# Kernel tuning notes

Hardware: AMD Instinct MI355X
Metric: run time of the kernel (lower is better)

Reference implementation:

```python
import jax, jax.numpy as jnp
import numpy as np

N_DIM = 128
M_SEQ = 2048
BATCH = 256


def setup_inputs() -> dict:
    key = jax.random.key(0)
    k1, k2, k3 = jax.random.split(key, 3)
    scale = 1.0 / np.sqrt(N_DIM)
    return {
        "x": jax.random.normal(k1, (BATCH, N_DIM, M_SEQ), dtype=jnp.float32),
        "W": jax.random.normal(k2, (N_DIM, 3 * N_DIM), dtype=jnp.float32) * scale,
        "U": jax.random.normal(k3, (N_DIM, 3 * N_DIM), dtype=jnp.float32) * scale,
        "b": jnp.zeros((3 * N_DIM,), dtype=jnp.float32),
    }


def reference(x, W, U, b):
    # x: [B, D, T] -> scan over T with a GRU cell, output [B, D, T]
    B, D, T = x.shape
    xs = jnp.transpose(x, (2, 0, 1))  # [T, B, D]

    def cell(h, xt):
        gx = xt @ W + b              # [B, 3D]
        gh = h @ U                   # [B, 3D]
        xz, xr, xn = jnp.split(gx, 3, axis=-1)
        hz, hr, hn = jnp.split(gh, 3, axis=-1)
        z = jax.nn.sigmoid(xz + hz)  # update gate
        r = jax.nn.sigmoid(xr + hr)  # reset gate
        n = jnp.tanh(xn + r * hn)    # candidate
        h_new = z * h + (1.0 - z) * n
        return h_new, h_new

    h0 = jnp.zeros((B, D), dtype=x.dtype)
    _, ys = jax.lax.scan(cell, h0, xs)   # ys: [T, B, D]
    return jnp.transpose(ys, (1, 2, 0))  # [B, D, T]
```

## Files before the change

kernel.cpp:

```cpp
#include <hip/hip_runtime.h>

typedef float f32x4 __attribute__((ext_vector_type(4)));
typedef short bf16x8 __attribute__((ext_vector_type(8)));

#define TT    2048
#define DDIM  128
#define G3    384
#define NBBLK 16
#define GXROW 6144
#define GX_BYTES ((size_t)NBBLK * TT * GXROW * 2)

#define SCL_ZR (-1.4426950408889634f)
#define SCL_N  (-2.8853900817779268f)

__device__ __forceinline__ unsigned f2bf_u(float f) {
    unsigned u = __float_as_uint(f);
    return (u + 0x7FFFu + ((u >> 16) & 1u)) >> 16;
}
__device__ __forceinline__ float bf_lo(unsigned u) { return __uint_as_float(u << 16); }
__device__ __forceinline__ float bf_hi(unsigned u) { return __uint_as_float(u & 0xffff0000u); }
__device__ __forceinline__ float rcp_(float x) { return __builtin_amdgcn_rcpf(x); }
__device__ __forceinline__ float exp2_(float x) {
    float d;
    asm("v_exp_f32 %0, %1" : "=v"(d) : "v"(x));
    return d;
}
__device__ __forceinline__ float sigm_(float v) { return rcp_(1.0f + exp2_(-1.4426950408889634f * v)); }
__device__ __forceinline__ float tanhf_(float v) { return 2.0f * rcp_(1.0f + exp2_(-2.8853900817779268f * v)) - 1.0f; }
__device__ __forceinline__ unsigned cvt_pk_bf16(float lo, float hi) {
    unsigned d;
    asm("v_cvt_pk_bf16_f32 %0, %1, %2" : "=v"(d) : "v"(lo), "v"(hi));
    return d;
}

__global__ __launch_bounds__(256) void gx_gemm(
    const float* __restrict__ x, const float* __restrict__ W,
    const float* __restrict__ bias, unsigned short* __restrict__ gx)
{
    const int bblk  = blockIdx.x;
    const int ttile = blockIdx.y;
    const int tid = threadIdx.x;
    const int w  = tid >> 6;
    const int l  = tid & 63;
    const int lc = l & 15;
    const int lk = l >> 4;

    __shared__ unsigned short xs[16 * 16 * DDIM];

    const int tiles[6] = {2*w, 2*w+1, 2*w+8, 2*w+9, 2*w+16, 2*w+17};

    bf16x8 wfrag[6][4];
    f32x4  binit[6];
    #pragma unroll
    for (int i6 = 0; i6 < 6; ++i6) {
        const float scl = (i6 >= 4) ? SCL_N : SCL_ZR;
        #pragma unroll
        for (int i = 0; i < 4; ++i)
            binit[i6][i] = bias[tiles[i6] * 16 + lk * 4 + i] * scl;
        #pragma unroll
        for (int kt = 0; kt < 4; ++kt) {
            bf16x8 f;
            #pragma unroll
            for (int jj = 0; jj < 8; ++jj) {
                const int k = kt * 32 + lk * 8 + jj;
                f[jj] = (short)f2bf_u(W[k * G3 + tiles[i6] * 16 + lc] * scl);
            }
            wfrag[i6][kt] = f;
        }
    }

    int inoff[4];
    #pragma unroll
    for (int kt = 0; kt < 4; ++kt)
        inoff[kt] = (lc * 256 + kt * 64 + lk * 16) ^ ((lc & 7) << 4);

    const float* xb = x + (size_t)bblk * 16 * DDIM * TT;
    const int t0blk = ttile * 128;
    const int tq = tid & 3;
    const int pbase = tid >> 2;

    for (int chunk = 0; chunk < 8; ++chunk) {
        __syncthreads();
        const int t0 = t0blk + chunk * 16 + tq * 4;
        #pragma unroll 4
        for (int pp = 0; pp < 32; ++pp) {
            const int p = pbase + pp * 64;
            const int r = p >> 7, d = p & 127;
            f32x4 v = *(const f32x4*)(xb + (size_t)p * TT + t0);
            char* bp = (char*)xs + (tq * 4) * 4096 + (((r * 128 + d) * 2) ^ ((r & 7) << 4));
            const unsigned pkA = cvt_pk_bf16(v[0], v[1]);
            const unsigned pkB = cvt_pk_bf16(v[2], v[3]);
            *(unsigned short*)(bp)         = (unsigned short)pkA;
            *(unsigned short*)(bp + 4096)  = (unsigned short)(pkA >> 16);
            *(unsigned short*)(bp + 8192)  = (unsigned short)pkB;
            *(unsigned short*)(bp + 12288) = (unsigned short)(pkB >> 16);
        }
        __syncthreads();

        for (int t = 0; t < 16; ++t) {
            bf16x8 a[4];
            #pragma unroll
            for (int kt = 0; kt < 4; ++kt)
                a[kt] = *(const bf16x8*)((const char*)xs + t * 4096 + inoff[kt]);

            const int tglob = t0blk + chunk * 16 + t;
            #pragma unroll
            for (int i6 = 0; i6 < 6; ++i6) {
                f32x4 acc = binit[i6];
                #pragma unroll
                for (int kt = 0; kt < 4; ++kt)
                    acc = __builtin_amdgcn_mfma_f32_16x16x32_bf16(wfrag[i6][kt], a[kt], acc, 0, 0, 0);
                unsigned p0 = cvt_pk_bf16(acc[0], acc[1]);
                unsigned p1 = cvt_pk_bf16(acc[2], acc[3]);
                const size_t off = (size_t)(bblk * TT + tglob) * GXROW
                                   + (size_t)(((tiles[i6] * 4 + lk) * 16 + lc) * 4);
                *(uint2*)(gx + off) = make_uint2(p0, p1);
            }
        }
    }
}

__global__ __launch_bounds__(512, 2) void gru_rec(
    const unsigned short* __restrict__ gx, const float* __restrict__ U,
    float* __restrict__ out)
{
    const int bblk = blockIdx.x;
    const int tid  = threadIdx.x;
    const int w  = tid >> 6;
    const int l  = tid & 63;
    const int lc = l & 15, lk = l >> 4;

    bf16x8 uz[4], ur[4], un[4];
    #pragma unroll
    for (int kt = 0; kt < 4; ++kt) {
        bf16x8 fz, fr, fn;
        #pragma unroll
        for (int jj = 0; jj < 8; ++jj) {
            const int k = kt * 32 + lk * 8 + jj;
            fz[jj] = (short)f2bf_u(U[k * G3 + (w * 16 + lc)] * SCL_ZR);
            fr[jj] = (short)f2bf_u(U[k * G3 + 128 + (w * 16 + lc)] * SCL_ZR);
            fn[jj] = (short)f2bf_u(U[k * G3 + 256 + (w * 16 + lc)] * SCL_N);
        }
        uz[kt] = fz; ur[kt] = fr; un[kt] = fn;
    }

    __shared__ unsigned short hsA[2 * 2048];
    __shared__ float hlds[16 * 16 * 128];
    #pragma unroll
    for (int i = tid; i < 4096; i += 512) hsA[i] = 0;
    char* const hb_lds = (char*)hlds;

    int roff[4];
    #pragma unroll
    for (int kt = 0; kt < 4; ++kt)
        roff[kt] = lc * 256 + ((kt * 64 + lk * 16) ^ (lc << 4));

    const int wb64 = lc * 256 + ((w * 32 + lk * 8) ^ (lc << 4));

    int hlv[4];
    {
        const int hlbase = lc * 512 + ((w * 64 + lk * 16) ^ ((lc & 7) << 4));
        #pragma unroll
        for (int s = 0; s < 4; ++s) hlv[s] = hlbase ^ (s << 6);
    }

    const int dl  = w * 16 + (l >> 2);
    const int qfl = l & 3;
    const int flb = qfl * 32768 + ((dl * 4) ^ (qfl << 6));
    float* outl = out + ((size_t)bblk * 16 * DDIM + dl) * TT + qfl * 4;

    float hold[4] = {0.f, 0.f, 0.f, 0.f};

    const unsigned short* g0 = gx + (size_t)bblk * TT * GXROW
                               + (size_t)(((w * 4 + lk) * 16 + lc) * 4);

    uint2 rgz[4], rgr[4], rgn[4];
    #pragma unroll
    for (int d = 0; d < 4; ++d) {
        const unsigned short* gq = g0 + (size_t)d * GXROW;
        rgz[d] = *(const uint2*)(gq);
        rgr[d] = *(const uint2*)(gq + 2048);
        rgn[d] = *(const uint2*)(gq + 4096);
    }

    __syncthreads();

#define GATE(I)                                                               \
    {                                                                         \
        const float zz = rcp_(1.0f + exp2_(az_a[I] + az_b[I]));               \
        const float rr = rcp_(1.0f + exp2_(ar_a[I] + ar_b[I]));               \
        const float uu = gn##I + rr * (an_a[I] + an_b[I]);                    \
        const float nn = 2.0f * rcp_(1.0f + exp2_(uu)) - 1.0f;                \
        const float hn = nn + zz * (hold[I] - nn);                            \
        hold[I] = hn;                                                         \
        hh[I] = hn;                                                           \
    }

#define SUBSTEP(J, DOPF)                                                      \
    {                                                                         \
        const char* hb = (const char*)hsA + ((J) & 1) * 4096;                 \
        bf16x8 b0 = *(const bf16x8*)(hb + roff[0]);                           \
        bf16x8 b1 = *(const bf16x8*)(hb + roff[1]);                           \
        bf16x8 b2 = *(const bf16x8*)(hb + roff[2]);                           \
        bf16x8 b3 = *(const bf16x8*)(hb + roff[3]);                           \
        uint2 pz = rgz[(J) & 3], pr = rgr[(J) & 3], pn = rgn[(J) & 3];        \
        if (DOPF) {                                                           \
            const unsigned short* gq = gpt + (size_t)((J) + 4) * GXROW;       \
            rgz[(J) & 3] = *(const uint2*)(gq);                               \
            rgr[(J) & 3] = *(const uint2*)(gq + 2048);                        \
            rgn[(J) & 3] = *(const uint2*)(gq + 4096);                        \
        }                                                                     \
        f32x4 az_a, ar_a;                                                     \
        az_a[0] = bf_lo(pz.x); az_a[1] = bf_hi(pz.x);                         \
        az_a[2] = bf_lo(pz.y); az_a[3] = bf_hi(pz.y);                         \
        ar_a[0] = bf_lo(pr.x); ar_a[1] = bf_hi(pr.x);                         \
        ar_a[2] = bf_lo(pr.y); ar_a[3] = bf_hi(pr.y);                         \
        const float gn0 = bf_lo(pn.x), gn1 = bf_hi(pn.x);                     \
        const float gn2 = bf_lo(pn.y), gn3 = bf_hi(pn.y);                     \
        f32x4 an_a = (f32x4){0.f, 0.f, 0.f, 0.f};                             \
        f32x4 an_b = an_a, az_b = an_a, ar_b = an_a;                          \
        an_a = __builtin_amdgcn_mfma_f32_16x16x32_bf16(un[0], b0, an_a, 0, 0, 0); \
        an_b = __builtin_amdgcn_mfma_f32_16x16x32_bf16(un[2], b2, an_b, 0, 0, 0); \
        az_a = __builtin_amdgcn_mfma_f32_16x16x32_bf16(uz[0], b0, az_a, 0, 0, 0); \
        az_b = __builtin_amdgcn_mfma_f32_16x16x32_bf16(uz[2], b2, az_b, 0, 0, 0); \
        ar_a = __builtin_amdgcn_mfma_f32_16x16x32_bf16(ur[0], b0, ar_a, 0, 0, 0); \
        ar_b = __builtin_amdgcn_mfma_f32_16x16x32_bf16(ur[2], b2, ar_b, 0, 0, 0); \
        an_a = __builtin_amdgcn_mfma_f32_16x16x32_bf16(un[1], b1, an_a, 0, 0, 0); \
        an_b = __builtin_amdgcn_mfma_f32_16x16x32_bf16(un[3], b3, an_b, 0, 0, 0); \
        az_a = __builtin_amdgcn_mfma_f32_16x16x32_bf16(uz[1], b1, az_a, 0, 0, 0); \
        az_b = __builtin_amdgcn_mfma_f32_16x16x32_bf16(uz[3], b3, az_b, 0, 0, 0); \
        ar_a = __builtin_amdgcn_mfma_f32_16x16x32_bf16(ur[1], b1, ar_a, 0, 0, 0); \
        ar_b = __builtin_amdgcn_mfma_f32_16x16x32_bf16(ur[3], b3, ar_b, 0, 0, 0); \
        float hh[4];                                                          \
        GATE(0) GATE(1) GATE(2) GATE(3)                                       \
        {                                                                     \
            const unsigned pk01 = cvt_pk_bf16(hh[0], hh[1]);                  \
            const unsigned pk23 = cvt_pk_bf16(hh[2], hh[3]);                  \
            *(uint2*)((char*)hsA + ((((J) & 1) ^ 1) * 4096) + wb64)           \
                = make_uint2(pk01, pk23);                                     \
        }                                                                     \
        *(f32x4*)(hb_lds + hlv[(J) >> 2] + (J) * 8192)                        \
            = (f32x4){hh[0], hh[1], hh[2], hh[3]};                            \
        asm volatile("s_waitcnt lgkmcnt(0)" ::: "memory");                    \
        __builtin_amdgcn_s_barrier();                                         \
    }

#define FLUSH(T0)                                                             \
    _Pragma("unroll")                                                         \
    for (int r = 0; r < 16; ++r) {                                            \
        const int fr = (flb ^ ((r & 7) << 4)) + r * 512;                      \
        f32x4 v;                                                              \
        _Pragma("unroll")                                                     \
        for (int k = 0; k < 4; ++k)                                           \
            v[k] = *(const float*)(hb_lds + fr + k * 8192);                   \
        *(f32x4*)(outl + (size_t)r * (DDIM * TT) + (T0)) = v;                 \
    }

    for (int t = 0; t < TT - 16; t += 16) {
        const unsigned short* gpt = g0 + (size_t)t * GXROW;
        SUBSTEP(0, true)  SUBSTEP(1, true)  SUBSTEP(2, true)  SUBSTEP(3, true)
        SUBSTEP(4, true)  SUBSTEP(5, true)  SUBSTEP(6, true)  SUBSTEP(7, true)
        SUBSTEP(8, true)  SUBSTEP(9, true)  SUBSTEP(10, true) SUBSTEP(11, true)
        SUBSTEP(12, true) SUBSTEP(13, true) SUBSTEP(14, true) SUBSTEP(15, true)
        FLUSH(t)
    }
    {
        const int t = TT - 16;
        const unsigned short* gpt = g0 + (size_t)t * GXROW;
        SUBSTEP(0, true)  SUBSTEP(1, true)  SUBSTEP(2, true)  SUBSTEP(3, true)
        SUBSTEP(4, true)  SUBSTEP(5, true)  SUBSTEP(6, true)  SUBSTEP(7, true)
        SUBSTEP(8, true)  SUBSTEP(9, true)  SUBSTEP(10, true) SUBSTEP(11, true)
        SUBSTEP(12, false) SUBSTEP(13, false) SUBSTEP(14, false) SUBSTEP(15, false)
        FLUSH(t)
    }
#undef GATE
#undef SUBSTEP
#undef FLUSH
}

typedef float f32x2 __attribute__((ext_vector_type(2)));

__global__ __launch_bounds__(768) void gru_fused(
    const float* __restrict__ x, const float* __restrict__ W,
    const float* __restrict__ U, const float* __restrict__ b,
    float* __restrict__ out)
{
    const int bb  = blockIdx.x;
    const int tid = threadIdx.x;
    const int kh  = (tid >= G3) ? 1 : 0;
    const int c   = tid - kh * G3;
    const int kbase = kh * 64;

    f32x2 wcol[32], ucol[32];
    #pragma unroll
    for (int k2 = 0; k2 < 32; ++k2) {
        wcol[k2][0] = W[(size_t)(kbase + 2*k2 + 0) * G3 + c];
        wcol[k2][1] = W[(size_t)(kbase + 2*k2 + 1) * G3 + c];
        ucol[k2][0] = U[(size_t)(kbase + 2*k2 + 0) * G3 + c];
        ucol[k2][1] = U[(size_t)(kbase + 2*k2 + 1) * G3 + c];
    }
    const float bias = b[c];

    __shared__ float xs[2][DDIM];
    __shared__ float hs[DDIM];
    __shared__ float px[G3], ph[G3];
    __shared__ float rs[DDIM], ns[DDIM];

    if (tid < DDIM) { hs[tid] = 0.0f; xs[0][tid] = x[((size_t)bb * DDIM + tid) * TT]; }
    __syncthreads();

    const float* __restrict__ xrow = x   + (size_t)bb * DDIM * TT;
    float* __restrict__       orow = out + (size_t)bb * DDIM * TT;
    float zv = 0.0f;

    for (int t = 0; t < TT; ++t) {
        const float* xcur = xs[t & 1] + kbase;
        const float* hcur = hs + kbase;
        f32x2 axv = {0.f, 0.f}, ahv = {0.f, 0.f};
        #pragma unroll
        for (int k2 = 0; k2 < 32; ++k2) {
            f32x2 xv = *(const f32x2*)(xcur + 2*k2);
            f32x2 hv = *(const f32x2*)(hcur + 2*k2);
            axv += xv * wcol[k2];
            ahv += hv * ucol[k2];
        }
        float ax = axv[0] + axv[1];
        float ah = ahv[0] + ahv[1];
        if (kh) { px[c] = ax; ph[c] = ah; }
        if (t + 1 < TT && tid >= 128 && tid < 256) {
            const int k = tid - 128;
            xs[(t + 1) & 1][k] = xrow[(size_t)k * TT + (t + 1)];
        }
        __syncthreads();
        if (!kh) {
            ax += px[c]; ah += ph[c];
            if (c < DDIM)            zv = sigm_(ax + ah + bias);
            else if (c < 2*DDIM)     rs[c - DDIM] = sigm_(ax + ah + bias);
            else { px[c] = ax + bias; ph[c] = ah; }
        }
        __syncthreads();
        if (!kh && c >= 2*DDIM) {
            float r = rs[c - 2*DDIM];
            ns[c - 2*DDIM] = tanhf_(px[c] + r * ph[c]);
        }
        __syncthreads();
        if (tid < DDIM) {
            float n = ns[tid];
            float hnew = zv * hs[tid] + (1.0f - zv) * n;
            hs[tid] = hnew;
            orow[(size_t)tid * TT + t] = hnew;
        }
        __syncthreads();
    }
}

extern "C" void kernel_launch(void* const* d_in, const int* in_sizes, int n_in,
                              void* d_out, int out_size, void* d_ws, size_t ws_size,
                              hipStream_t stream) {
    const float* x = (const float*)d_in[0];
    const float* W = (const float*)d_in[1];
    const float* U = (const float*)d_in[2];
    const float* b = (const float*)d_in[3];
    float* out     = (float*)d_out;

    if (ws_size >= GX_BYTES) {
        unsigned short* gx = (unsigned short*)d_ws;
        hipLaunchKernelGGL(gx_gemm, dim3(16, 16), dim3(256), 0, stream, x, W, b, gx);
        hipLaunchKernelGGL(gru_rec, dim3(16), dim3(512), 0, stream, gx, U, out);
    } else {
        hipLaunchKernelGGL(gru_fused, dim3(256), dim3(768), 0, stream, x, W, U, b, out);
    }
}
```

Measured before the change: 1.676 ms.

## Pack two batch blocks per 1024-thread workgroup and flush output every 8 steps

The recurrent kernel now runs two independent 16-row batch blocks in one 1024-thread workgroup, each half with its own LDS hidden-state and staging buffers, launched as 8 workgroups instead of 16. The output staging buffer is halved and flushed every 8 timesteps instead of 16, and the fp32 staging store moves after the barrier. Because the two halves share one s_barrier, each timestep's barrier now synchronises 16 waves, which may add stall time. The changed output-index and swizzle mapping is also a correctness risk.

```diff
diff --git a/kernel.cpp b/kernel.cpp
--- a/kernel.cpp
+++ b/kernel.cpp
@@ -120,15 +120,17 @@
     }
 }
 
-__global__ __launch_bounds__(512, 2) void gru_rec(
+__global__ __launch_bounds__(1024) void gru_rec(
     const unsigned short* __restrict__ gx, const float* __restrict__ U,
     float* __restrict__ out)
 {
-    const int bblk = blockIdx.x;
     const int tid  = threadIdx.x;
-    const int w  = tid >> 6;
-    const int l  = tid & 63;
+    const int half = tid >> 9;
+    const int t2   = tid & 511;
+    const int w  = t2 >> 6;
+    const int l  = t2 & 63;
     const int lc = l & 15, lk = l >> 4;
+    const int bblk = blockIdx.x * 2 + half;
 
     bf16x8 uz[4], ur[4], un[4];
     #pragma unroll
@@ -144,11 +146,12 @@
         uz[kt] = fz; ur[kt] = fr; un[kt] = fn;
     }
 
-    __shared__ unsigned short hsA[2 * 2048];
-    __shared__ float hlds[16 * 16 * 128];
-    #pragma unroll
-    for (int i = tid; i < 4096; i += 512) hsA[i] = 0;
-    char* const hb_lds = (char*)hlds;
+    __shared__ unsigned short hsA[2][2 * 2048];
+    __shared__ float hlds[2][8 * 16 * 128];
+    #pragma unroll
+    for (int i = t2; i < 4096; i += 512) hsA[half][i] = 0;
+    char* const hsA_h  = (char*)&hsA[half][0];
+    char* const hb_lds = (char*)&hlds[half][0];
 
     int roff[4];
     #pragma unroll
@@ -157,17 +160,19 @@
 
     const int wb64 = lc * 256 + ((w * 32 + lk * 8) ^ (lc << 4));
 
-    int hlv[4];
+    int hlv[2];
     {
-        const int hlbase = lc * 512 + ((w * 64 + lk * 16) ^ ((lc & 7) << 4));
-        #pragma unroll
-        for (int s = 0; s < 4; ++s) hlv[s] = hlbase ^ (s << 6);
+        const int base = lc * 512 + ((w * 64 + lk * 16) ^ ((lc & 7) << 4));
+        hlv[0] = base;
+        hlv[1] = 32768 + (base ^ (1 << 6));
     }
 
     const int dl  = w * 16 + (l >> 2);
-    const int qfl = l & 3;
-    const int flb = qfl * 32768 + ((dl * 4) ^ (qfl << 6));
-    float* outl = out + ((size_t)bblk * 16 * DDIM + dl) * TT + qfl * 4;
+    const int bh  = (l & 3) >> 1;
+    const int q   = l & 1;
+    const int flA = ((dl * 4) ^ (q << 6)) + q * 32768;
+    float* outfl = out + (size_t)(bblk * 16 + 8 * bh) * DDIM * TT + (size_t)dl * TT + q * 16/4*4;
+    float* outq = out + ((size_t)(bblk * 16 + 8 * bh) * DDIM + dl) * TT + q * 4;
 
     float hold[4] = {0.f, 0.f, 0.f, 0.f};
 
@@ -198,7 +203,7 @@
 
 #define SUBSTEP(J, DOPF)                                                      \
     {                                                                         \
-        const char* hb = (const char*)hsA + ((J) & 1) * 4096;                 \
+        const char* hb = hsA_h + ((J) & 1) * 4096;                            \
         bf16x8 b0 = *(const bf16x8*)(hb + roff[0]);                           \
         bf16x8 b1 = *(const bf16x8*)(hb + roff[1]);                           \
         bf16x8 b2 = *(const bf16x8*)(hb + roff[2]);                           \
@@ -236,46 +241,47 @@
         {                                                                     \
             const unsigned pk01 = cvt_pk_bf16(hh[0], hh[1]);                  \
             const unsigned pk23 = cvt_pk_bf16(hh[2], hh[3]);                  \
-            *(uint2*)((char*)hsA + ((((J) & 1) ^ 1) * 4096) + wb64)           \
+            *(uint2*)(hsA_h + ((((J) & 1) ^ 1) * 4096) + wb64)                \
                 = make_uint2(pk01, pk23);                                     \
         }                                                                     \
-        *(f32x4*)(hb_lds + hlv[(J) >> 2] + (J) * 8192)                        \
-            = (f32x4){hh[0], hh[1], hh[2], hh[3]};                            \
         asm volatile("s_waitcnt lgkmcnt(0)" ::: "memory");                    \
         __builtin_amdgcn_s_barrier();                                         \
+         \
+         \
+        *(f32x4*)(hb_lds + hlv[(J) >> 2] + ((J) & 3) * 8192)                  \
+            = (f32x4){hh[0], hh[1], hh[2], hh[3]};                            \
     }
 
 #define FLUSH(T0)                                                             \
+    asm volatile("s_waitcnt lgkmcnt(0)" ::: "memory");                        \
     _Pragma("unroll")                                                         \
-    for (int r = 0; r < 16; ++r) {                                            \
-        const int fr = (flb ^ ((r & 7) << 4)) + r * 512;                      \
+    for (int r = 0; r < 8; ++r) {                                             \
+        const int b_ = r + 8 * bh;                                            \
+        const int fr = q * 32768 + b_ * 512 + (((dl * 4) ^ ((b_ & 7) << 4)) ^ (q << 6)); \
         f32x4 v;                                                              \
         _Pragma("unroll")                                                     \
         for (int k = 0; k < 4; ++k)                                           \
             v[k] = *(const float*)(hb_lds + fr + k * 8192);                   \
-        *(f32x4*)(outl + (size_t)r * (DDIM * TT) + (T0)) = v;                 \
-    }
-
-    for (int t = 0; t < TT - 16; t += 16) {
+        *(f32x4*)(outq + (size_t)r * (DDIM * TT) + (T0)) = v;                 \
+    }
+
+    for (int t = 0; t < TT - 8; t += 8) {
+        const unsigned short* gpt = g0 + (size_t)t * GXROW;
+        SUBSTEP(0, true) SUBSTEP(1, true) SUBSTEP(2, true) SUBSTEP(3, true)
+        SUBSTEP(4, true) SUBSTEP(5, true) SUBSTEP(6, true) SUBSTEP(7, true)
+        FLUSH(t)
+    }
+    {
+        const int t = TT - 8;
         const unsigned short* gpt = g0 + (size_t)t * GXROW;
         SUBSTEP(0, true)  SUBSTEP(1, true)  SUBSTEP(2, true)  SUBSTEP(3, true)
-        SUBSTEP(4, true)  SUBSTEP(5, true)  SUBSTEP(6, true)  SUBSTEP(7, true)
-        SUBSTEP(8, true)  SUBSTEP(9, true)  SUBSTEP(10, true) SUBSTEP(11, true)
-        SUBSTEP(12, true) SUBSTEP(13, true) SUBSTEP(14, true) SUBSTEP(15, true)
-        FLUSH(t)
-    }
-    {
-        const int t = TT - 16;
-        const unsigned short* gpt = g0 + (size_t)t * GXROW;
-        SUBSTEP(0, true)  SUBSTEP(1, true)  SUBSTEP(2, true)  SUBSTEP(3, true)
-        SUBSTEP(4, true)  SUBSTEP(5, true)  SUBSTEP(6, true)  SUBSTEP(7, true)
-        SUBSTEP(8, true)  SUBSTEP(9, true)  SUBSTEP(10, true) SUBSTEP(11, true)
-        SUBSTEP(12, false) SUBSTEP(13, false) SUBSTEP(14, false) SUBSTEP(15, false)
+        SUBSTEP(4, false) SUBSTEP(5, false) SUBSTEP(6, false) SUBSTEP(7, false)
         FLUSH(t)
     }
 #undef GATE
 #undef SUBSTEP
 #undef FLUSH
+    (void)outfl;
 }
 
 typedef float f32x2 __attribute__((ext_vector_type(2)));
@@ -366,7 +372,7 @@
     if (ws_size >= GX_BYTES) {
         unsigned short* gx = (unsigned short*)d_ws;
         hipLaunchKernelGGL(gx_gemm, dim3(16, 16), dim3(256), 0, stream, x, W, b, gx);
-        hipLaunchKernelGGL(gru_rec, dim3(16), dim3(512), 0, stream, gx, U, out);
+        hipLaunchKernelGGL(gru_rec, dim3(8), dim3(1024), 0, stream, gx, U, out);
     } else {
         hipLaunchKernelGGL(gru_fused, dim3(256), dim3(768), 0, stream, x, W, U, b, out);
     }
```

New measurement: 3.054 ms. +82.2%, slower.
